# Kernel tuning notes

Measured on AMD Instinct MI355X. Metric: run time of the kernel, lower is better.

Reference implementation:

```python
import jax, jax.numpy as jnp
import numpy as np

L, N, E, H = 2048, 2, 1024, 16
D = E // H  # head dim = 64


def setup_inputs() -> dict:
    key = jax.random.key(0)
    k1, k2, k3, k4, k5 = jax.random.split(key, 5)
    s = 1.0 / np.sqrt(E)
    return {
        "x": jax.random.normal(k1, (L, N, E), dtype=jnp.float32),
        "in_proj_weight": jax.random.normal(k2, (3 * E, E), dtype=jnp.float32) * s,
        "in_proj_bias": jax.random.normal(k3, (3 * E,), dtype=jnp.float32) * 0.01,
        "out_proj_weight": jax.random.normal(k4, (E, E), dtype=jnp.float32) * s,
        "out_proj_bias": jax.random.normal(k5, (E,), dtype=jnp.float32) * 0.01,
    }


def reference(x, in_proj_weight, in_proj_bias, out_proj_weight, out_proj_bias):
    # packed qkv in-projection: (L, N, 3E)
    qkv = jnp.einsum("lne,fe->lnf", x, in_proj_weight) + in_proj_bias
    q, k, v = jnp.split(qkv, 3, axis=-1)

    def heads(t):  # (L, N, E) -> (N, H, L, D)
        return t.reshape(L, N, H, D).transpose(1, 2, 0, 3)

    q, k, v = heads(q), heads(k), heads(v)
    scale = 1.0 / jnp.sqrt(jnp.asarray(D, dtype=q.dtype))
    scores = jnp.einsum("nhld,nhmd->nhlm", q * scale, k)  # (N, H, L, L)
    attn = jax.nn.softmax(scores, axis=-1)
    out = jnp.einsum("nhlm,nhmd->nhld", attn, v)  # (N, H, L, D)
    out = out.transpose(2, 0, 1, 3).reshape(L, N, E)
    return jnp.einsum("lne,fe->lnf", out, out_proj_weight) + out_proj_bias
```

## Files before the change

### kernel.cpp

```cpp
#include <hip/hip_runtime.h>

typedef __attribute__((ext_vector_type(8))) short bf16x8;
typedef __attribute__((ext_vector_type(4))) float f32x4;
typedef __attribute__((ext_vector_type(16))) float f32x16;
typedef __attribute__((ext_vector_type(8))) unsigned short ushort8;
typedef __attribute__((ext_vector_type(4))) unsigned short ushort4_t;
typedef __attribute__((ext_vector_type(4))) unsigned uint4_t;

#define LSEQ 2048
#define NB 2
#define EMB 1024
#define NHEAD 16
#define HD 64

__device__ __forceinline__ unsigned short f2bf(float f) {
  unsigned u = __builtin_bit_cast(unsigned, f);
  u += 0x7fffu + ((u >> 16) & 1u);
  return (unsigned short)(u >> 16);
}
__device__ __forceinline__ float bf2f(unsigned short s) {
  return __builtin_bit_cast(float, ((unsigned)s) << 16);
}

__device__ __forceinline__ void gll16(const void* g, void* l) {
  __builtin_amdgcn_global_load_lds((const __attribute__((address_space(1))) unsigned*)g,
                                   (__attribute__((address_space(3))) unsigned*)l, 16, 0, 0);
}

__global__ __launch_bounds__(256) void cvt_f32_bf16(const float* __restrict__ in,
                                                    unsigned short* __restrict__ out, int n4) {
  int i = blockIdx.x * 256 + threadIdx.x;
  if (i >= n4) return;
  float4 v = ((const float4*)in)[i];
  ushort4_t o;
  o.x = f2bf(v.x); o.y = f2bf(v.y); o.z = f2bf(v.z); o.w = f2bf(v.w);
  ((ushort4_t*)out)[i] = o;
}

template <bool OUT_BF16>
__global__ __launch_bounds__(256, 2) void gemm_bf16_nt(
    const unsigned short* __restrict__ A, const unsigned short* __restrict__ B,
    const float* __restrict__ bias, void* __restrict__ Cout, int M, int Ncol, int K) {
  __shared__ unsigned short Asm[128 * 64];
  __shared__ unsigned short Bsm[128 * 64];
  const int tid = threadIdx.x;
  const int wave = tid >> 6, lane = tid & 63;
  const int wr = (wave >> 1) * 64, wc = (wave & 1) * 64;
  const int lr = lane & 15, lg = lane >> 4;
  const int bm = blockIdx.x * 128, bn = blockIdx.y * 128;

  f32x4 acc[4][4];
#pragma unroll
  for (int i = 0; i < 4; ++i)
#pragma unroll
    for (int j = 0; j < 4; ++j) acc[i][j] = (f32x4){0.f, 0.f, 0.f, 0.f};

  for (int kt = 0; kt < K; kt += 64) {
#pragma unroll
    for (int c = 0; c < 4; ++c) {
      int idx = (c * 4 + wave) * 64 + lane;
      int row = idx >> 3, ch = (idx & 7) * 8;
      gll16(A + (size_t)(bm + row) * K + kt + ch, &Asm[(c * 4 + wave) * 512]);
      gll16(B + (size_t)(bn + row) * K + kt + ch, &Bsm[(c * 4 + wave) * 512]);
    }
    __syncthreads();
#pragma unroll
    for (int ks = 0; ks < 2; ++ks) {
      bf16x8 af[4], bfr[4];
#pragma unroll
      for (int i = 0; i < 4; ++i)
        af[i] = *(const bf16x8*)&Asm[(wr + i * 16 + lr) * 64 + ks * 32 + lg * 8];
#pragma unroll
      for (int j = 0; j < 4; ++j)
        bfr[j] = *(const bf16x8*)&Bsm[(wc + j * 16 + lr) * 64 + ks * 32 + lg * 8];
#pragma unroll
      for (int i = 0; i < 4; ++i)
#pragma unroll
        for (int j = 0; j < 4; ++j)
          acc[i][j] = __builtin_amdgcn_mfma_f32_16x16x32_bf16(af[i], bfr[j], acc[i][j], 0, 0, 0);
    }
    __syncthreads();
  }
#pragma unroll
  for (int i = 0; i < 4; ++i) {
#pragma unroll
    for (int j = 0; j < 4; ++j) {
      int col = bn + wc + j * 16 + lr;
      float bv = bias[col];
#pragma unroll
      for (int r = 0; r < 4; ++r) {
        int row = bm + wr + i * 16 + lg * 4 + r;
        float v = acc[i][j][r] + bv;
        if constexpr (OUT_BF16)
          ((unsigned short*)Cout)[(size_t)row * Ncol + col] = f2bf(v);
        else
          ((float*)Cout)[(size_t)row * Ncol + col] = v;
      }
    }
  }
}

__global__ __launch_bounds__(256) void transpose_v(const unsigned short* __restrict__ qkv,
                                                   unsigned short* __restrict__ vt) {
  __shared__ unsigned short t[64][72];
  const int nh = blockIdx.y, n = nh >> 4, h = nh & 15;
  const int lt = blockIdx.x * 64;
  const int tid = threadIdx.x;
#pragma unroll
  for (int it = 0; it < 2; ++it) {
    int idx = it * 256 + tid;
    int l = idx >> 3, ch = (idx & 7) * 8;
    ushort8 v = *(const ushort8*)(qkv + (size_t)((lt + l) * NB + n) * 3072 + 2 * EMB + h * HD + ch);
    *(ushort8*)&t[l][ch] = v;
  }
  __syncthreads();
  int d = tid >> 2, lc = (tid & 3) * 16;
  unsigned short tmp[16];
#pragma unroll
  for (int i = 0; i < 16; ++i) tmp[i] = t[lc + i][d];
#pragma unroll
  for (int i = 0; i < 2; ++i)
    *(ushort8*)(vt + (size_t)(nh * HD + d) * LSEQ + lt + lc + i * 8) = *(const ushort8*)&tmp[i * 8];
}

__global__ __launch_bounds__(256, 3) void flash_attn(const unsigned short* __restrict__ qkv,
                                                     const unsigned short* __restrict__ vt,
                                                     unsigned short* __restrict__ ob) {
  __shared__ unsigned short Ksm[2][64 * 64];
  __shared__ unsigned short Vsm[2][64 * 64];
  const int tid = threadIdx.x, wave = tid >> 6, lane = tid & 63;
  const int l31 = lane & 31, lh = lane >> 5;
  const int flat = blockIdx.y * 16 + blockIdx.x;
  const int fb = (flat & 7) * 64 + (flat >> 3);
  const int nh = fb >> 4, qt = fb & 15;
  const int n = nh >> 4, hh = nh & 15;
  const int q = qt * 128 + wave * 32 + l31;

  const int sch = ((lane & 7) ^ ((lane >> 3) & 7)) * 8;
  const unsigned short* Kbase = qkv + (size_t)n * 3072 + EMB + hh * HD + sch;
  const unsigned short* Vbase = vt + (size_t)nh * HD * LSEQ + sch;

  bf16x8 qf[4];
  {
    const unsigned short* qb = qkv + ((size_t)q * NB + n) * 3072 + hh * HD + lh * 8;
#pragma unroll
    for (int t = 0; t < 4; ++t) {
      bf16x8 tv = *(const bf16x8*)(qb + t * 16);
#pragma unroll
      for (int e = 0; e < 8; ++e)
        tv[e] = (short)f2bf(bf2f((unsigned short)tv[e]) * 0.18033688f);
      qf[t] = tv;
    }
  }

  auto stage = [&](int buf, int kt) {
#pragma unroll
    for (int c = 0; c < 2; ++c) {
      int row = ((c * 4 + wave) * 64 + lane) >> 3;
      gll16(Kbase + (size_t)(kt * 64 + row) * (NB * 3072), &Ksm[buf][(c * 4 + wave) * 512]);
      gll16(Vbase + (size_t)row * LSEQ + kt * 64, &Vsm[buf][(c * 4 + wave) * 512]);
    }
  };

  float m = -1e30f, lsum = 0.f;
  f32x16 o0, o1;
#pragma unroll
  for (int r = 0; r < 16; ++r) { o0[r] = 0.f; o1[r] = 0.f; }

  stage(0, 0);
  __syncthreads();
  int cur = 0;
  const int swz = l31 & 7;

  for (int kt = 0; kt < LSEQ / 64; ++kt) {
    if (kt < LSEQ / 64 - 1) stage(cur ^ 1, kt + 1);

    f32x16 s0, s1;
#pragma unroll
    for (int r = 0; r < 16; ++r) { s0[r] = 0.f; s1[r] = 0.f; }
    __builtin_amdgcn_s_setprio(1);
#pragma unroll
    for (int t = 0; t < 4; ++t) {
      int ch = ((t * 2 + lh) ^ swz) * 8;
      bf16x8 k0 = *(const bf16x8*)&Ksm[cur][l31 * 64 + ch];
      bf16x8 k1 = *(const bf16x8*)&Ksm[cur][(32 + l31) * 64 + ch];
      s0 = __builtin_amdgcn_mfma_f32_32x32x16_bf16(k0, qf[t], s0, 0, 0, 0);
      s1 = __builtin_amdgcn_mfma_f32_32x32x16_bf16(k1, qf[t], s1, 0, 0, 0);
    }
    __builtin_amdgcn_s_setprio(0);

    float mx = fmaxf(s0[0], s1[0]);
#pragma unroll
    for (int r = 1; r < 16; ++r) mx = fmaxf(mx, fmaxf(s0[r], s1[r]));
    mx = fmaxf(mx, __shfl_xor(mx, 32));
    float mn = fmaxf(m, mx);
    float al = exp2f(m - mn);
    m = mn;
    float ps = 0.f;
#pragma unroll
    for (int r = 0; r < 16; ++r) {
      float p0 = exp2f(s0[r] - mn), p1 = exp2f(s1[r] - mn);
      s0[r] = p0; s1[r] = p1;
      ps += p0 + p1;
    }
    ps += __shfl_xor(ps, 32);
    lsum = lsum * al + ps;
#pragma unroll
    for (int r = 0; r < 16; ++r) { o0[r] *= al; o1[r] *= al; }

    bf16x8 pf[4];
#pragma unroll
    for (int g = 0; g < 4; ++g) {
      const int b = (g & 1) * 8;
      float a0 = (g < 2) ? s0[b + 0] : s1[b + 0];
      float a1 = (g < 2) ? s0[b + 1] : s1[b + 1];
      float a2 = (g < 2) ? s0[b + 2] : s1[b + 2];
      float a3 = (g < 2) ? s0[b + 3] : s1[b + 3];
      float a4 = (g < 2) ? s0[b + 4] : s1[b + 4];
      float a5 = (g < 2) ? s0[b + 5] : s1[b + 5];
      float a6 = (g < 2) ? s0[b + 6] : s1[b + 6];
      float a7 = (g < 2) ? s0[b + 7] : s1[b + 7];
      unsigned w0, w1, w2, w3;
      asm("v_cvt_pk_bf16_f32 %0, %1, %2" : "=v"(w0) : "v"(a0), "v"(a1));
      asm("v_cvt_pk_bf16_f32 %0, %1, %2" : "=v"(w1) : "v"(a2), "v"(a3));
      asm("v_cvt_pk_bf16_f32 %0, %1, %2" : "=v"(w2) : "v"(a4), "v"(a5));
      asm("v_cvt_pk_bf16_f32 %0, %1, %2" : "=v"(w3) : "v"(a6), "v"(a7));
      asm("v_permlane32_swap_b32 %0, %1" : "+v"(w0), "+v"(w2));
      asm("v_permlane32_swap_b32 %0, %1" : "+v"(w1), "+v"(w3));
      pf[g] = __builtin_bit_cast(bf16x8, (uint4_t){w0, w1, w2, w3});
    }

    __builtin_amdgcn_s_setprio(1);
#pragma unroll
    for (int u = 0; u < 4; ++u) {
      int ch = ((u * 2 + lh) ^ swz) * 8;
      bf16x8 a0 = *(const bf16x8*)&Vsm[cur][l31 * 64 + ch];
      bf16x8 a1 = *(const bf16x8*)&Vsm[cur][(32 + l31) * 64 + ch];
      o0 = __builtin_amdgcn_mfma_f32_32x32x16_bf16(a0, pf[u], o0, 0, 0, 0);
      o1 = __builtin_amdgcn_mfma_f32_32x32x16_bf16(a1, pf[u], o1, 0, 0, 0);
    }
    __builtin_amdgcn_s_setprio(0);

    __syncthreads();
    cur ^= 1;
  }

  float inv = 1.0f / lsum;
  unsigned short* op = ob + ((size_t)q * NB + n) * EMB + hh * HD;
#pragma unroll
  for (int g = 0; g < 4; ++g) {
    ushort4_t pk0, pk1;
#pragma unroll
    for (int e = 0; e < 4; ++e) {
      pk0[e] = f2bf(o0[g * 4 + e] * inv);
      pk1[e] = f2bf(o1[g * 4 + e] * inv);
    }
    *(ushort4_t*)(op + g * 8 + lh * 4) = pk0;
    *(ushort4_t*)(op + 32 + g * 8 + lh * 4) = pk1;
  }
}

extern "C" void kernel_launch(void* const* d_in, const int* in_sizes, int n_in,
                              void* d_out, int out_size, void* d_ws, size_t ws_size,
                              hipStream_t stream) {
  const float* x = (const float*)d_in[0];
  const float* wqkv = (const float*)d_in[1];
  const float* bqkv = (const float*)d_in[2];
  const float* wout = (const float*)d_in[3];
  const float* bout = (const float*)d_in[4];

  char* ws = (char*)d_ws;
  unsigned short* xb    = (unsigned short*)(ws);
  unsigned short* wqkvb = (unsigned short*)(ws + 8388608);
  unsigned short* woutb = (unsigned short*)(ws + 14680064);
  unsigned short* qkvb  = (unsigned short*)(ws + 16777216);
  unsigned short* vtb   = (unsigned short*)(ws + 41943040);
  unsigned short* obuf  = (unsigned short*)(ws + 50331648);

  cvt_f32_bf16<<<4096, 256, 0, stream>>>(x, xb, 1048576);
  cvt_f32_bf16<<<3072, 256, 0, stream>>>(wqkv, wqkvb, 786432);
  cvt_f32_bf16<<<1024, 256, 0, stream>>>(wout, woutb, 262144);

  dim3 g1(32, 24);
  gemm_bf16_nt<true><<<g1, 256, 0, stream>>>(xb, wqkvb, bqkv, qkvb, 4096, 3072, 1024);

  dim3 gt(32, 32);
  transpose_v<<<gt, 256, 0, stream>>>(qkvb, vtb);

  dim3 g2(16, 32);
  flash_attn<<<g2, 256, 0, stream>>>(qkvb, vtb, obuf);

  dim3 g3(32, 8);
  gemm_bf16_nt<false><<<g3, 256, 0, stream>>>(obuf, woutb, bout, d_out, 4096, 1024, 1024);
}
```

Before: 223.7 us.

## Widen attention KV tile to 128, add lazy rescaling, fuse conversion kernels

The flash attention loop now processes 128 keys per iteration instead of 64, which doubles the shared-memory K/V buffers and drops the occupancy hint from 3 to 2 blocks. The V staging swizzle is adapted to 128-wide rows. Row max uses v_max3, and the output rescale is skipped when the new max exceeds the running max by at most 8 (in the log2 domain), so fewer exp/multiply operations run per tile. The three fp32-to-bf16 conversion launches are merged into one kernel to cut launch overhead. The trade-off is higher register and LDS pressure, which lowers occupancy.

```diff
diff --git a/kernel.cpp b/kernel.cpp
--- a/kernel.cpp
+++ b/kernel.cpp
@@ -21,20 +21,34 @@
 __device__ __forceinline__ float bf2f(unsigned short s) {
   return __builtin_bit_cast(float, ((unsigned)s) << 16);
 }
+__device__ __forceinline__ float vmax3(float a, float b, float c) {
+  float d;
+  asm("v_max3_f32 %0, %1, %2, %3" : "=v"(d) : "v"(a), "v"(b), "v"(c));
+  return d;
+}
 
 __device__ __forceinline__ void gll16(const void* g, void* l) {
   __builtin_amdgcn_global_load_lds((const __attribute__((address_space(1))) unsigned*)g,
                                    (__attribute__((address_space(3))) unsigned*)l, 16, 0, 0);
 }
 
-__global__ __launch_bounds__(256) void cvt_f32_bf16(const float* __restrict__ in,
-                                                    unsigned short* __restrict__ out, int n4) {
+__global__ __launch_bounds__(256) void cvt_all(const float* __restrict__ x,
+                                               const float* __restrict__ wq,
+                                               const float* __restrict__ wo,
+                                               unsigned short* __restrict__ xb,
+                                               unsigned short* __restrict__ wqb,
+                                               unsigned short* __restrict__ wob) {
   int i = blockIdx.x * 256 + threadIdx.x;
-  if (i >= n4) return;
-  float4 v = ((const float4*)in)[i];
+  const float* src;
+  unsigned short* dst;
+  int off;
+  if (i < 1048576) { src = x;  dst = xb;  off = i; }
+  else if (i < 1835008) { src = wq; dst = wqb; off = i - 1048576; }
+  else { src = wo; dst = wob; off = i - 1835008; }
+  float4 v = ((const float4*)src)[off];
   ushort4_t o;
   o.x = f2bf(v.x); o.y = f2bf(v.y); o.z = f2bf(v.z); o.w = f2bf(v.w);
-  ((ushort4_t*)out)[i] = o;
+  ((ushort4_t*)dst)[off] = o;
 }
 
 template <bool OUT_BF16>
@@ -123,11 +137,11 @@
     *(ushort8*)(vt + (size_t)(nh * HD + d) * LSEQ + lt + lc + i * 8) = *(const ushort8*)&tmp[i * 8];
 }
 
-__global__ __launch_bounds__(256, 3) void flash_attn(const unsigned short* __restrict__ qkv,
+__global__ __launch_bounds__(256, 2) void flash_attn(const unsigned short* __restrict__ qkv,
                                                      const unsigned short* __restrict__ vt,
                                                      unsigned short* __restrict__ ob) {
-  __shared__ unsigned short Ksm[2][64 * 64];
-  __shared__ unsigned short Vsm[2][64 * 64];
+  __shared__ unsigned short Ksm[2][128 * 64];
+  __shared__ unsigned short Vsm[2][64 * 128];
   const int tid = threadIdx.x, wave = tid >> 6, lane = tid & 63;
   const int l31 = lane & 31, lh = lane >> 5;
   const int flat = blockIdx.y * 16 + blockIdx.x;
@@ -138,7 +152,7 @@
 
   const int sch = ((lane & 7) ^ ((lane >> 3) & 7)) * 8;
   const unsigned short* Kbase = qkv + (size_t)n * 3072 + EMB + hh * HD + sch;
-  const unsigned short* Vbase = vt + (size_t)nh * HD * LSEQ + sch;
+  const size_t vbase = (size_t)nh * HD * LSEQ;
 
   bf16x8 qf[4];
   {
@@ -155,10 +169,13 @@
 
   auto stage = [&](int buf, int kt) {
 #pragma unroll
-    for (int c = 0; c < 2; ++c) {
-      int row = ((c * 4 + wave) * 64 + lane) >> 3;
-      gll16(Kbase + (size_t)(kt * 64 + row) * (NB * 3072), &Ksm[buf][(c * 4 + wave) * 512]);
-      gll16(Vbase + (size_t)row * LSEQ + kt * 64, &Vsm[buf][(c * 4 + wave) * 512]);
+    for (int c = 0; c < 4; ++c) {
+      int cc = c * 4 + wave;
+      int krow = cc * 8 + (lane >> 3);
+      gll16(Kbase + (size_t)(kt * 128 + krow) * (NB * 3072), &Ksm[buf][cc * 512]);
+      int vrow = cc * 4 + (lane >> 4);
+      int schv = ((lane & 15) ^ ((cc & 1) * 4 + (lane >> 4))) * 8;
+      gll16(vt + vbase + (size_t)vrow * LSEQ + kt * 128 + schv, &Vsm[buf][cc * 512]);
     }
   };
 
@@ -172,70 +189,98 @@
   int cur = 0;
   const int swz = l31 & 7;
 
-  for (int kt = 0; kt < LSEQ / 64; ++kt) {
-    if (kt < LSEQ / 64 - 1) stage(cur ^ 1, kt + 1);
-
-    f32x16 s0, s1;
-#pragma unroll
-    for (int r = 0; r < 16; ++r) { s0[r] = 0.f; s1[r] = 0.f; }
+  for (int kt = 0; kt < LSEQ / 128; ++kt) {
+    if (kt < LSEQ / 128 - 1) stage(cur ^ 1, kt + 1);
+
+    f32x16 s[4];
+#pragma unroll
+    for (int kb = 0; kb < 4; ++kb)
+#pragma unroll
+      for (int r = 0; r < 16; ++r) s[kb][r] = 0.f;
     __builtin_amdgcn_s_setprio(1);
 #pragma unroll
     for (int t = 0; t < 4; ++t) {
       int ch = ((t * 2 + lh) ^ swz) * 8;
-      bf16x8 k0 = *(const bf16x8*)&Ksm[cur][l31 * 64 + ch];
-      bf16x8 k1 = *(const bf16x8*)&Ksm[cur][(32 + l31) * 64 + ch];
-      s0 = __builtin_amdgcn_mfma_f32_32x32x16_bf16(k0, qf[t], s0, 0, 0, 0);
-      s1 = __builtin_amdgcn_mfma_f32_32x32x16_bf16(k1, qf[t], s1, 0, 0, 0);
+#pragma unroll
+      for (int kb = 0; kb < 4; ++kb) {
+        bf16x8 kf = *(const bf16x8*)&Ksm[cur][(kb * 32 + l31) * 64 + ch];
+        s[kb] = __builtin_amdgcn_mfma_f32_32x32x16_bf16(kf, qf[t], s[kb], 0, 0, 0);
+      }
     }
     __builtin_amdgcn_s_setprio(0);
 
-    float mx = fmaxf(s0[0], s1[0]);
-#pragma unroll
-    for (int r = 1; r < 16; ++r) mx = fmaxf(mx, fmaxf(s0[r], s1[r]));
+    f32x16 mv;
+#pragma unroll
+    for (int r = 0; r < 16; ++r) mv[r] = vmax3(s[0][r], s[1][r], s[2][r]);
+#pragma unroll
+    for (int r = 0; r < 16; ++r) mv[r] = fmaxf(mv[r], s[3][r]);
+    float t0 = vmax3(mv[0], mv[1], mv[2]);
+    float t1 = vmax3(mv[3], mv[4], mv[5]);
+    float t2 = vmax3(mv[6], mv[7], mv[8]);
+    float t3 = vmax3(mv[9], mv[10], mv[11]);
+    float t4 = vmax3(mv[12], mv[13], mv[14]);
+    float mx = fmaxf(vmax3(t0, t1, t2), vmax3(t3, t4, mv[15]));
     mx = fmaxf(mx, __shfl_xor(mx, 32));
-    float mn = fmaxf(m, mx);
-    float al = exp2f(m - mn);
-    m = mn;
-    float ps = 0.f;
-#pragma unroll
-    for (int r = 0; r < 16; ++r) {
-      float p0 = exp2f(s0[r] - mn), p1 = exp2f(s1[r] - mn);
-      s0[r] = p0; s1[r] = p1;
-      ps += p0 + p1;
-    }
+
+    if (!__all(mx - m <= 8.0f)) {
+      float mn = fmaxf(m, mx);
+      float al = exp2f(m - mn);
+      lsum *= al;
+#pragma unroll
+      for (int r = 0; r < 16; ++r) { o0[r] *= al; o1[r] *= al; }
+      m = mn;
+    }
+
+    float ps0 = 0.f, ps1 = 0.f, ps2 = 0.f, ps3 = 0.f;
+#pragma unroll
+    for (int kb = 0; kb < 4; ++kb) {
+#pragma unroll
+      for (int r = 0; r < 16; r += 4) {
+        float p0 = exp2f(s[kb][r] - m);
+        float p1 = exp2f(s[kb][r + 1] - m);
+        float p2 = exp2f(s[kb][r + 2] - m);
+        float p3 = exp2f(s[kb][r + 3] - m);
+        s[kb][r] = p0; s[kb][r + 1] = p1; s[kb][r + 2] = p2; s[kb][r + 3] = p3;
+        ps0 += p0; ps1 += p1; ps2 += p2; ps3 += p3;
+      }
+    }
+    float ps = (ps0 + ps1) + (ps2 + ps3);
     ps += __shfl_xor(ps, 32);
-    lsum = lsum * al + ps;
-#pragma unroll
-    for (int r = 0; r < 16; ++r) { o0[r] *= al; o1[r] *= al; }
-
-    bf16x8 pf[4];
-#pragma unroll
-    for (int g = 0; g < 4; ++g) {
-      const int b = (g & 1) * 8;
-      float a0 = (g < 2) ? s0[b + 0] : s1[b + 0];
-      float a1 = (g < 2) ? s0[b + 1] : s1[b + 1];
-      float a2 = (g < 2) ? s0[b + 2] : s1[b + 2];
-      float a3 = (g < 2) ? s0[b + 3] : s1[b + 3];
-      float a4 = (g < 2) ? s0[b + 4] : s1[b + 4];
-      float a5 = (g < 2) ? s0[b + 5] : s1[b + 5];
-      float a6 = (g < 2) ? s0[b + 6] : s1[b + 6];
-      float a7 = (g < 2) ? s0[b + 7] : s1[b + 7];
-      unsigned w0, w1, w2, w3;
-      asm("v_cvt_pk_bf16_f32 %0, %1, %2" : "=v"(w0) : "v"(a0), "v"(a1));
-      asm("v_cvt_pk_bf16_f32 %0, %1, %2" : "=v"(w1) : "v"(a2), "v"(a3));
-      asm("v_cvt_pk_bf16_f32 %0, %1, %2" : "=v"(w2) : "v"(a4), "v"(a5));
-      asm("v_cvt_pk_bf16_f32 %0, %1, %2" : "=v"(w3) : "v"(a6), "v"(a7));
-      asm("v_permlane32_swap_b32 %0, %1" : "+v"(w0), "+v"(w2));
-      asm("v_permlane32_swap_b32 %0, %1" : "+v"(w1), "+v"(w3));
-      pf[g] = __builtin_bit_cast(bf16x8, (uint4_t){w0, w1, w2, w3});
+    lsum += ps;
+
+    bf16x8 pf[8];
+#pragma unroll
+    for (int half = 0; half < 2; ++half) {
+      const f32x16& sa = s[half * 2];
+      const f32x16& sb = s[half * 2 + 1];
+#pragma unroll
+      for (int g = 0; g < 4; ++g) {
+        const int b = (g & 1) * 8;
+        float a0 = (g < 2) ? sa[b + 0] : sb[b + 0];
+        float a1 = (g < 2) ? sa[b + 1] : sb[b + 1];
+        float a2 = (g < 2) ? sa[b + 2] : sb[b + 2];
+        float a3 = (g < 2) ? sa[b + 3] : sb[b + 3];
+        float a4 = (g < 2) ? sa[b + 4] : sb[b + 4];
+        float a5 = (g < 2) ? sa[b + 5] : sb[b + 5];
+        float a6 = (g < 2) ? sa[b + 6] : sb[b + 6];
+        float a7 = (g < 2) ? sa[b + 7] : sb[b + 7];
+        unsigned w0, w1, w2, w3;
+        asm("v_cvt_pk_bf16_f32 %0, %1, %2" : "=v"(w0) : "v"(a0), "v"(a1));
+        asm("v_cvt_pk_bf16_f32 %0, %1, %2" : "=v"(w1) : "v"(a2), "v"(a3));
+        asm("v_cvt_pk_bf16_f32 %0, %1, %2" : "=v"(w2) : "v"(a4), "v"(a5));
+        asm("v_cvt_pk_bf16_f32 %0, %1, %2" : "=v"(w3) : "v"(a6), "v"(a7));
+        asm("v_permlane32_swap_b32 %0, %1" : "+v"(w0), "+v"(w2));
+        asm("v_permlane32_swap_b32 %0, %1" : "+v"(w1), "+v"(w3));
+        pf[half * 4 + g] = __builtin_bit_cast(bf16x8, (uint4_t){w0, w1, w2, w3});
+      }
     }
 
     __builtin_amdgcn_s_setprio(1);
 #pragma unroll
-    for (int u = 0; u < 4; ++u) {
+    for (int u = 0; u < 8; ++u) {
       int ch = ((u * 2 + lh) ^ swz) * 8;
-      bf16x8 a0 = *(const bf16x8*)&Vsm[cur][l31 * 64 + ch];
-      bf16x8 a1 = *(const bf16x8*)&Vsm[cur][(32 + l31) * 64 + ch];
+      bf16x8 a0 = *(const bf16x8*)&Vsm[cur][l31 * 128 + ch];
+      bf16x8 a1 = *(const bf16x8*)&Vsm[cur][(32 + l31) * 128 + ch];
       o0 = __builtin_amdgcn_mfma_f32_32x32x16_bf16(a0, pf[u], o0, 0, 0, 0);
       o1 = __builtin_amdgcn_mfma_f32_32x32x16_bf16(a1, pf[u], o1, 0, 0, 0);
     }
@@ -277,9 +322,7 @@
   unsigned short* vtb   = (unsigned short*)(ws + 41943040);
   unsigned short* obuf  = (unsigned short*)(ws + 50331648);
 
-  cvt_f32_bf16<<<4096, 256, 0, stream>>>(x, xb, 1048576);
-  cvt_f32_bf16<<<3072, 256, 0, stream>>>(wqkv, wqkvb, 786432);
-  cvt_f32_bf16<<<1024, 256, 0, stream>>>(wout, woutb, 262144);
+  cvt_all<<<8192, 256, 0, stream>>>(x, wqkv, wout, xb, wqkvb, woutb);
 
   dim3 g1(32, 24);
   gemm_bf16_nt<true><<<g1, 256, 0, stream>>>(xb, wqkvb, bqkv, qkvb, 4096, 3072, 1024);
```

After: 211.5 us. 5.4% less time.
